# Optimization experiments

Measured on AMD Instinct MI355X. Metric: run time of the kernel, lower is better.

## Reference

```python
import jax, jax.numpy as jnp
import numpy as np

N_UE, N_AP, K = 8192, 2048, 3          # dst nodes, src nodes, neighbors per dst (graphlet_size-1)
E = N_UE * K
D_NODE, D_EDGE, H = 8, 4, 128          # raw feature dims, hidden_dim
PQC_DIM, PQC_OUT, NCLS = 2, 3, 2
NQ = 9                                  # 3 edge wires + 4 node wires (center=wire 3) + 2 ancilla (7,8)
CENTER = 3
C64 = jnp.complex64
X_GATE = jnp.array([[0.0, 1.0], [1.0, 0.0]], dtype=C64)


def RXm(t):
    c = jnp.cos(0.5 * t).astype(C64)
    s = (-1j * jnp.sin(0.5 * t)).astype(C64)
    return jnp.stack([jnp.stack([c, s]), jnp.stack([s, c])])


def RYm(t):
    c, s = jnp.cos(0.5 * t), jnp.sin(0.5 * t)
    return jnp.stack([jnp.stack([c, -s]), jnp.stack([s, c])]).astype(C64)


def RZm(t):
    e = jnp.exp(-0.5j * t.astype(C64))
    z = jnp.zeros_like(e)
    return jnp.stack([jnp.stack([e, z]), jnp.stack([z, jnp.conj(e)])])


def ROTm(phi, theta, omega):  # qml.Rot = RZ(omega) @ RY(theta) @ RZ(phi)
    return RZm(omega) @ RYm(theta) @ RZm(phi)


def ap1(psi, U, w):  # apply 1-qubit gate on wire w
    psi = jnp.tensordot(U, psi, axes=([1], [w]))
    return jnp.moveaxis(psi, 0, w)


def apc(psi, U, c, t):  # controlled-U, control c, target t
    G = jnp.zeros((4, 4), C64).at[:2, :2].set(jnp.eye(2, dtype=C64)).at[2:, 2:].set(U)
    psi = jnp.tensordot(G.reshape(2, 2, 2, 2), psi, axes=([2, 3], [c, t]))
    return jnp.moveaxis(psi, (0, 1), (c, t))


def sel(psi, w, wires):  # qml.StronglyEntanglingLayers, w: (L, M, 3)
    L, M = w.shape[0], len(wires)
    for l in range(L):
        for j, q in enumerate(wires):
            psi = ap1(psi, ROTm(w[l, j, 0], w[l, j, 1], w[l, j, 2]), q)
        r = l % (M - 1) + 1  # pennylane default ranges
        for j in range(M):
            psi = apc(psi, X_GATE, wires[j], wires[(j + r) % M])
    return psi


def expz(psi, w):  # <PauliZ(w)>
    p = psi.real ** 2 + psi.imag ** 2
    m = p.sum(axis=tuple(a for a in range(NQ) if a != w))
    return m[0] - m[1]


def circuit(flat, strong, inits, update):  # qgcn_enhance_layer, flat: (14,)
    inp = flat.reshape(7, 2)
    ef, nf = inp[:3], inp[3:]  # 3 edge rows, then center + 3 neighbor rows
    psi = jnp.zeros((2,) * NQ, C64).at[(0,) * NQ].set(1.0)
    for i in range(3):  # edge feature encoding
        psi = ap1(psi, RXm(ef[i, 0]), i)
        psi = ap1(psi, RZm(ef[i, 1]), i)
    for i in range(4):  # node feature encoding (center on wire 3)
        psi = ap1(psi, RXm(nf[i, 0]), CENTER + i)
        psi = ap1(psi, RZm(nf[i, 1]), CENTER + i)
    for i in range(3):  # message_passing_pqc per edge
        e, nb = i, CENTER + i + 1
        psi = apc(psi, RXm(inits[0, 0]), nb, e)
        psi = apc(psi, RYm(inits[0, 1]), e, nb)
        psi = sel(psi, strong[0], [e, nb])
    for i in range(3):  # update entanglers over center/neighbor/ancilla
        psi = sel(psi, update[i], [CENTER, CENTER + i + 1, 7, 8])
    return jnp.stack([expz(psi, CENTER), expz(psi, 7), expz(psi, 8)])


def mlp2(x, W1, b1, W2, b2):  # PyG MLP in eval mode; BatchNorm at default stats == identity
    return jax.nn.leaky_relu(x @ W1 + b1) @ W2 + b2


def _forward(x_ue, x_ap, edge_attr,
             Wn1u, bn1u, Wn2u, bn2u, Wn1a, bn1a, Wn2a, bn2a,
             We1, be1, We2, be2, strong, inits, update,
             Wu1, bu1, Wu2, bu2, ln_g, ln_b,
             Wf1, bf1, Wf2, bf2, Wf3, bf3, edge_src):
    ue = mlp2(x_ue, Wn1u, bn1u, Wn2u, bn2u)        # (N_UE, 2)  input_node['UE']
    ap = mlp2(x_ap, Wn1a, bn1a, Wn2a, bn2a)        # (N_AP, 2)  input_node['AP']
    ea = mlp2(edge_attr, We1, be1, We2, be2)       # (E, 2)     input_edge['UE']
    nbrs = ap[edge_src].reshape(N_UE, K, PQC_DIM)  # neighbor gather (K per dst)
    ef = ea.reshape(N_UE, K, PQC_DIM)              # edges grouped by dst: edge_dst = repeat(arange(N_UE), K)
    flat = jnp.concatenate([ef, ue[:, None, :], nbrs], axis=1).reshape(N_UE, 14)
    msg = jax.vmap(lambda f: circuit(f, strong, inits, update))(flat)  # (N_UE, 3)
    upd = mlp2(jnp.concatenate([ue, msg], axis=-1), Wu1, bu1, Wu2, bu2)  # (N_UE, 2)
    h = ue + upd  # index_add scatter: each dst updated exactly once
    mu = h.mean(-1, keepdims=True)
    var = h.var(-1, keepdims=True)
    h = (h - mu) / jnp.sqrt(var + 1e-5) * ln_g + ln_b  # LayerNorm(2)
    h = jax.nn.leaky_relu(h @ Wf1 + bf1)
    h = jax.nn.leaky_relu(h @ Wf2 + bf2)
    return jax.nn.sigmoid(h @ Wf3 + bf3)  # (N_UE, NCLS)


def setup_inputs() -> dict:
    ks = jax.random.split(jax.random.key(0), 20)

    def rn(i, shape, s=0.2):
        return jax.random.normal(ks[i], shape, jnp.float32) * s

    def qw(i, shape):  # uniform_pi_init
        return jax.random.uniform(ks[i], shape, jnp.float32, 0.0, np.pi)

    return dict(
        x_ue=jax.random.normal(ks[0], (N_UE, D_NODE), jnp.float32),
        x_ap=jax.random.normal(ks[1], (N_AP, D_NODE), jnp.float32),
        edge_attr=jax.random.normal(ks[2], (E, D_EDGE), jnp.float32),
        edge_src=jax.random.randint(ks[3], (E,), 0, N_AP),
        edge_dst=jnp.repeat(jnp.arange(N_UE), K),
        Wn1u=rn(4, (D_NODE, H)), bn1u=jnp.zeros((H,), jnp.float32),
        Wn2u=rn(5, (H, PQC_DIM)), bn2u=jnp.zeros((PQC_DIM,), jnp.float32),
        Wn1a=rn(6, (D_NODE, H)), bn1a=jnp.zeros((H,), jnp.float32),
        Wn2a=rn(7, (H, PQC_DIM)), bn2a=jnp.zeros((PQC_DIM,), jnp.float32),
        We1=rn(8, (D_EDGE, H)), be1=jnp.zeros((H,), jnp.float32),
        We2=rn(9, (H, PQC_DIM)), be2=jnp.zeros((PQC_DIM,), jnp.float32),
        strong=qw(10, (1, 2, 2, 3)), inits=qw(11, (1, 2)), update=qw(12, (3, 2, 4, 3)),
        Wu1=rn(13, (PQC_DIM + PQC_OUT, H)), bu1=jnp.zeros((H,), jnp.float32),
        Wu2=rn(14, (H, PQC_DIM)), bu2=jnp.zeros((PQC_DIM,), jnp.float32),
        ln_g=jnp.ones((PQC_DIM,), jnp.float32), ln_b=jnp.zeros((PQC_DIM,), jnp.float32),
        Wf1=rn(15, (PQC_DIM, H)), bf1=jnp.zeros((H,), jnp.float32),
        Wf2=rn(16, (H, H)), bf2=jnp.zeros((H,), jnp.float32),
        Wf3=rn(17, (H, NCLS)), bf3=jnp.zeros((NCLS,), jnp.float32),
    )


def reference(x_ue, x_ap, edge_attr, edge_src, edge_dst,
              Wn1u, bn1u, Wn2u, bn2u, Wn1a, bn1a, Wn2a, bn2a,
              We1, be1, We2, be2, strong, inits, update,
              Wu1, bu1, Wu2, bu2, ln_g, ln_b,
              Wf1, bf1, Wf2, bf2, Wf3, bf3):
    del edge_dst  # edges are constructed grouped per dst; grouping realized via reshape
    return _forward(x_ue, x_ap, edge_attr,
                    Wn1u, bn1u, Wn2u, bn2u, Wn1a, bn1a, Wn2a, bn2a,
                    We1, be1, We2, be2, strong, inits, update,
                    Wu1, bu1, Wu2, bu2, ln_g, ln_b,
                    Wf1, bf1, Wf2, bf2, Wf3, bf3, edge_src)
```

## Files before the change

kernel.cpp:

```cpp
#include <hip/hip_runtime.h>

#define LEAKY(x) ((x) > 0.0f ? (x) : 0.01f * (x))

#define GP_F    672
#define APE     2208
#define UEE     6304
#define EAE     22688
#define G_F     71840

__device__ __forceinline__ float2 cmul(float2 a, float2 b) {
  return make_float2(fmaf(a.x, b.x, -a.y * b.y), fmaf(a.x, b.y, a.y * b.x));
}
__device__ __forceinline__ float2 cmulc(float2 a, float2 b) {
  return make_float2(fmaf(a.x, b.x, a.y * b.y), fmaf(a.x, b.y, -a.y * b.x));
}
__device__ __forceinline__ float2 cadd(float2 a, float2 b) {
  return make_float2(a.x + b.x, a.y + b.y);
}
__device__ __forceinline__ float2 csub(float2 a, float2 b) {
  return make_float2(a.x - b.x, a.y - b.y);
}
__device__ __forceinline__ void swap2(float2& a, float2& b) {
  float2 t = a; a = b; b = t;
}

struct C2 { float2 e[4]; };

__device__ C2 cmm(const C2& A, const C2& B) {
  C2 R;
  #pragma unroll
  for (int r = 0; r < 2; ++r)
    #pragma unroll
    for (int c = 0; c < 2; ++c)
      R.e[r*2+c] = cadd(cmul(A.e[r*2+0], B.e[0*2+c]), cmul(A.e[r*2+1], B.e[1*2+c]));
  return R;
}
__device__ C2 gRX(float t) {
  float s = __sinf(0.5f*t), c = __cosf(0.5f*t);
  C2 M;
  M.e[0] = make_float2(c, 0.f);  M.e[1] = make_float2(0.f, -s);
  M.e[2] = make_float2(0.f, -s); M.e[3] = make_float2(c, 0.f);
  return M;
}
__device__ C2 gRY(float t) {
  float s = __sinf(0.5f*t), c = __cosf(0.5f*t);
  C2 M;
  M.e[0] = make_float2(c, 0.f);  M.e[1] = make_float2(-s, 0.f);
  M.e[2] = make_float2(s, 0.f);  M.e[3] = make_float2(c, 0.f);
  return M;
}
__device__ C2 gRZ(float t) {
  float s = __sinf(0.5f*t), c = __cosf(0.5f*t);
  C2 M;
  M.e[0] = make_float2(c, -s);    M.e[1] = make_float2(0.f, 0.f);
  M.e[2] = make_float2(0.f, 0.f); M.e[3] = make_float2(c, s);
  return M;
}
__device__ C2 gROT(float phi, float th, float om) {
  return cmm(cmm(gRZ(om), gRY(th)), gRZ(phi));
}

template<int D>
__device__ __forceinline__ void encode_block(
    const float* __restrict__ x, int r,
    const float* __restrict__ W1, const float* __restrict__ b1,
    const float* __restrict__ W2, const float* __restrict__ b2,
    float* w1t, float* b1s, float* w2s, float* __restrict__ outp, int tid) {
  #pragma unroll
  for (int i = 0; i < D/2; ++i) {
    const int idx = i*256 + tid;
    const float v = W1[idx];
    w1t[(idx & 127)*D + (idx >> 7)] = v;
  }
  if (tid < 128) b1s[tid] = b1[tid];
  w2s[tid] = W2[tid];
  __syncthreads();

  float xv[D];
  *(float4*)xv = *(const float4*)(x + r*D);
  if (D == 8) *(float4*)(xv + 4) = *(const float4*)(x + r*D + 4);

  float o0 = 0.f, o1 = 0.f;
  #pragma unroll 4
  for (int j = 0; j < 128; ++j) {
    float h = b1s[j];
    #pragma unroll
    for (int k = 0; k < D; k += 4) {
      const float4 w = *(const float4*)&w1t[j*D + k];
      h = fmaf(xv[k],   w.x, h);
      h = fmaf(xv[k+1], w.y, h);
      h = fmaf(xv[k+2], w.z, h);
      h = fmaf(xv[k+3], w.w, h);
    }
    h = LEAKY(h);
    const float2 w2 = *(const float2*)&w2s[j*2];
    o0 = fmaf(h, w2.x, o0);
    o1 = fmaf(h, w2.y, o1);
  }
  *(float2*)(outp + r*2) = make_float2(o0 + b2[0], o1 + b2[1]);
}

__global__ __launch_bounds__(256) void enc_kernel(
    const float* __restrict__ x_ue, const float* __restrict__ x_ap,
    const float* __restrict__ edge_attr,
    const float* __restrict__ Wn1u, const float* __restrict__ bn1u,
    const float* __restrict__ Wn2u, const float* __restrict__ bn2u,
    const float* __restrict__ Wn1a, const float* __restrict__ bn1a,
    const float* __restrict__ Wn2a, const float* __restrict__ bn2a,
    const float* __restrict__ We1,  const float* __restrict__ be1,
    const float* __restrict__ We2,  const float* __restrict__ be2,
    const float* __restrict__ strongp, const float* __restrict__ initsp,
    const float* __restrict__ updatep, float* __restrict__ ws) {
  __shared__ __align__(16) float w1t[1024];
  __shared__ float b1s[128];
  __shared__ __align__(8) float w2s[256];
  __shared__ float2 U2s[16][17];
  const int bi = blockIdx.x, tid = threadIdx.x;

  if (bi < 32) {
    encode_block<8>(x_ue, bi*256 + tid, Wn1u, bn1u, Wn2u, bn2u,
                    w1t, b1s, w2s, ws + UEE, tid);
    return;
  } else if (bi < 40) {
    encode_block<8>(x_ap, (bi-32)*256 + tid, Wn1a, bn1a, Wn2a, bn2a,
                    w1t, b1s, w2s, ws + APE, tid);
    return;
  } else if (bi < 136) {
    encode_block<4>(edge_attr, (bi-40)*256 + tid, We1, be1, We2, be2,
                    w1t, b1s, w2s, ws + EAE, tid);
    return;
  }

  if (tid < 48) {
    const int k = tid >> 4, col = tid & 15;
    float2 u[16];
    #pragma unroll
    for (int r = 0; r < 16; ++r) u[r] = make_float2(r == col ? 1.f : 0.f, 0.f);
    #pragma unroll
    for (int l = 0; l < 2; ++l) {
      #pragma unroll
      for (int j = 0; j < 4; ++j) {
        const float* p = updatep + k*24 + l*12 + j*3;
        C2 U = gROT(p[0], p[1], p[2]);
        const int m = 8 >> j;
        #pragma unroll
        for (int r = 0; r < 16; ++r)
          if (!(r & m)) {
            float2 a0 = u[r], a1 = u[r | m];
            u[r]     = cadd(cmul(U.e[0], a0), cmul(U.e[1], a1));
            u[r | m] = cadd(cmul(U.e[2], a0), cmul(U.e[3], a1));
          }
      }
      #pragma unroll
      for (int j = 0; j < 4; ++j) {
        const int mc = 8 >> j;
        const int mt0[4] = {4, 2, 1, 8};
        const int mt1[4] = {2, 1, 8, 4};
        const int mt = (l == 0) ? mt0[j] : mt1[j];
        #pragma unroll
        for (int r = 0; r < 16; ++r)
          if ((r & mc) && !(r & mt)) swap2(u[r], u[r | mt]);
      }
    }
    if (k == 0) {
      if (!(col & 3)) {
        const int jc = col >> 2;
        #pragma unroll
        for (int r = 0; r < 16; ++r) {
          ws[32 + (jc*16 + r)*2 + 0] = u[r].x;
          ws[32 + (jc*16 + r)*2 + 1] = u[r].y;
        }
      }
    } else if (k == 1) {
      #pragma unroll
      for (int r = 0; r < 16; ++r) {
        ws[160 + (col*16 + r)*2 + 0] = u[r].x;
        ws[160 + (col*16 + r)*2 + 1] = u[r].y;
      }
    } else {
      #pragma unroll
      for (int r = 0; r < 16; ++r) U2s[col][r] = u[r];
    }
  }
  if (tid == 48) {
    float2 M[4][4];
    #pragma unroll
    for (int r = 0; r < 4; ++r)
      #pragma unroll
      for (int c = 0; c < 4; ++c)
        M[r][c] = make_float2(r == c ? 1.f : 0.f, 0.f);
    auto rowpair = [&](int r0, int r1, C2 U) {
      #pragma unroll
      for (int c = 0; c < 4; ++c) {
        float2 a0 = M[r0][c], a1 = M[r1][c];
        M[r0][c] = cadd(cmul(U.e[0], a0), cmul(U.e[1], a1));
        M[r1][c] = cadd(cmul(U.e[2], a0), cmul(U.e[3], a1));
      }
    };
    auto rowswap = [&](int r0, int r1) {
      #pragma unroll
      for (int c = 0; c < 4; ++c) swap2(M[r0][c], M[r1][c]);
    };
    rowpair(1, 3, gRX(initsp[0]));
    rowpair(2, 3, gRY(initsp[1]));
    #pragma unroll
    for (int l = 0; l < 2; ++l) {
      C2 Re = gROT(strongp[l*6+0], strongp[l*6+1], strongp[l*6+2]);
      C2 Rn = gROT(strongp[l*6+3], strongp[l*6+4], strongp[l*6+5]);
      rowpair(0, 2, Re); rowpair(1, 3, Re);
      rowpair(0, 1, Rn); rowpair(2, 3, Rn);
      rowswap(2, 3);
      rowswap(1, 3);
    }
    #pragma unroll
    for (int r = 0; r < 4; ++r)
      #pragma unroll
      for (int c = 0; c < 4; ++c) {
        ws[(r*4 + c)*2 + 0] = M[r][c].x;
        ws[(r*4 + c)*2 + 1] = M[r][c].y;
      }
  }
  __syncthreads();
  {
    const int c = tid >> 5, cp = (tid >> 2) & 7, n = (tid >> 1) & 1, np = tid & 1;
    const int q  = ((c  & 4) << 1) | (n  << 2) | (c  & 3);
    const int qp = ((cp & 4) << 1) | (np << 2) | (cp & 3);
    float2 g3 = make_float2(0,0), g7 = g3, g8 = g3;
    #pragma unroll
    for (int t = 0; t < 16; ++t) {
      float2 pr = cmulc(U2s[q][t], U2s[qp][t]);
      g3 = (t & 8) ? csub(g3, pr) : cadd(g3, pr);
      g7 = (t & 2) ? csub(g7, pr) : cadd(g7, pr);
      g8 = (t & 1) ? csub(g8, pr) : cadd(g8, pr);
    }
    const int idx = (c*2 + n)*16 + (cp*2 + np);
    ws[GP_F + (0*256 + idx)*2 + 0] = g3.x;
    ws[GP_F + (0*256 + idx)*2 + 1] = g3.y;
    ws[GP_F + (1*256 + idx)*2 + 0] = g7.x;
    ws[GP_F + (1*256 + idx)*2 + 1] = g7.y;
    ws[GP_F + (2*256 + idx)*2 + 0] = g8.x;
    ws[GP_F + (2*256 + idx)*2 + 1] = g8.y;
  }
}

__global__ __launch_bounds__(256) void circuit_kernel(
    float* __restrict__ ws, const int* __restrict__ esrc,
    const float* __restrict__ Wu1, const float* __restrict__ bu1,
    const float* __restrict__ Wu2, const float* __restrict__ bu2,
    const float* __restrict__ lng, const float* __restrict__ lnb) {
  __shared__ __align__(16) float2 cst[1104];
  __shared__ __align__(16) float2 pr_s[4][3][4];
  __shared__ __align__(16) float2 psi0[4][2][16];
  __shared__ __align__(16) float2 psi2[4][8][16];
  const int tid = threadIdx.x, wv = tid >> 6, lane = tid & 63;
  const int u = blockIdx.x*4 + wv;

  {
    const float4* s4 = (const float4*)ws;
    float4* d4 = (float4*)cst;
    #pragma unroll
    for (int i = tid; i < 552; i += 256) d4[i] = s4[i];
  }
  __syncthreads();

  const float2* MEl  = cst;
  const float2* U0cl = cst + 16;
  const float2* U1tl = cst + 80;
  const float2* GPl  = cst + 336;

  auto mkv = [](float aa, float bb, float2& v0, float2& v1) {
    const float sa = __sinf(0.5f*aa), ca = __cosf(0.5f*aa);
    const float sb = __sinf(0.5f*bb), cb = __cosf(0.5f*bb);
    v0 = make_float2(cb*ca, -sb*ca);
    v1 = make_float2(sa*sb, -sa*cb);
  };
  const float2 ue_ab = *(const float2*)(ws + UEE + u*2);
  float2 t0, t1;
  mkv(ue_ab.x, ue_ab.y, t0, t1);

  if (lane < 12) {
    const int i = lane >> 2, r = lane & 3;
    const float2 eab = *(const float2*)(ws + EAE + (u*3 + i)*2);
    const int s = esrc[u*3 + i];
    const float2 nab = *(const float2*)(ws + APE + s*2);
    float2 e0, e1, n0, n1;
    mkv(eab.x, eab.y, e0, e1);
    mkv(nab.x, nab.y, n0, n1);
    float2 in4[4] = {cmul(e0,n0), cmul(e0,n1), cmul(e1,n0), cmul(e1,n1)};
    float2 acc = make_float2(0.f, 0.f);
    #pragma unroll
    for (int cc = 0; cc < 4; ++cc) acc = cadd(acc, cmul(MEl[r*4 + cc], in4[cc]));
    pr_s[wv][i][r] = acc;
  }

  if (lane < 32) {
    const int b = lane >> 4, row = lane & 15;
    float2 acc = make_float2(0.f, 0.f);
    #pragma unroll
    for (int j = 0; j < 4; ++j) {
      const float2 phi = pr_s[wv][0][(b << 1) | (j & 1)];
      const float2 coef = cmul((j >> 1) ? t1 : t0, phi);
      acc = cadd(acc, cmul(U0cl[j*16 + row], coef));
    }
    psi0[wv][b][row] = acc;
  }

  {
    const int ibr = lane >> 3, rp = lane & 7;
    const int db = ibr >> 2, da = (ibr >> 1) & 1, dbp = ibr & 1;
    const float2 f10 = pr_s[wv][1][(dbp << 1) | 0];
    const float2 f11 = pr_s[wv][1][(dbp << 1) | 1];
    float2 chi[8];
    {
      const float4 a0 = *(const float4*)&psi0[wv][db][da*4 + 0];
      const float4 a1 = *(const float4*)&psi0[wv][db][da*4 + 2];
      const float4 a2 = *(const float4*)&psi0[wv][db][8 + da*4 + 0];
      const float4 a3 = *(const float4*)&psi0[wv][db][8 + da*4 + 2];
      chi[0] = make_float2(a0.x, a0.y); chi[1] = make_float2(a0.z, a0.w);
      chi[2] = make_float2(a1.x, a1.y); chi[3] = make_float2(a1.z, a1.w);
      chi[4] = make_float2(a2.x, a2.y); chi[5] = make_float2(a2.z, a2.w);
      chi[6] = make_float2(a3.x, a3.y); chi[7] = make_float2(a3.z, a3.w);
    }
    float2 q0 = make_float2(0.f, 0.f), q1 = q0;
    #pragma unroll
    for (int q = 0; q < 16; ++q) {
      const int cc = ((q >> 3) << 2) | (q & 3);
      const float2 xq = cmul(chi[cc], (q & 4) ? f11 : f10);
      q0 = cadd(q0, cmul(U1tl[q*16 + rp],     xq));
      q1 = cadd(q1, cmul(U1tl[q*16 + rp + 8], xq));
    }
    psi2[wv][ibr][rp]     = q0;
    psi2[wv][ibr][rp + 8] = q1;
  }

  const int c = lane >> 3, cp = lane & 7;
  const int mc0 = ((c  & 4) << 1) | (c  & 3);
  const int mp0 = ((cp & 4) << 1) | (cp & 3);
  float2 R = make_float2(0.f, 0.f);
  #pragma unroll
  for (int br = 0; br < 8; ++br) {
    const float2 z10 = psi2[wv][br][mc0], z11 = psi2[wv][br][mc0 + 4];
    const float2 z20 = psi2[wv][br][mp0], z21 = psi2[wv][br][mp0 + 4];
    R.x += z10.x*z20.x + z10.y*z20.y + z11.x*z21.x + z11.y*z21.y;
    R.y += z10.y*z20.x - z10.x*z20.y + z11.y*z21.x - z11.x*z21.y;
  }

  const float4 f2a = *(const float4*)&pr_s[wv][2][0];
  const float4 f2b = *(const float4*)&pr_s[wv][2][2];
  const float2 f20 = make_float2(f2a.x, f2a.y), f21 = make_float2(f2a.z, f2a.w);
  const float2 f22 = make_float2(f2b.x, f2b.y), f23 = make_float2(f2b.z, f2b.w);
  const float2 rho00 = make_float2(f20.x*f20.x + f20.y*f20.y + f22.x*f22.x + f22.y*f22.y, 0.f);
  const float2 rho11 = make_float2(f21.x*f21.x + f21.y*f21.y + f23.x*f23.x + f23.y*f23.y, 0.f);
  const float2 rho01 = make_float2(fmaf(f20.x,f21.x,f20.y*f21.y) + fmaf(f22.x,f23.x,f22.y*f23.y),
                                   (f20.y*f21.x - f20.x*f21.y) + (f22.y*f23.x - f22.x*f23.y));
  const float2 rho10 = make_float2(rho01.x, -rho01.y);

  float ev0, ev1, ev2;
  {
    const int base = (c*2)*16 + (cp*2);
    #pragma unroll
    for (int w = 0; w < 3; ++w) {
      const float2 g00 = GPl[w*256 + base];
      const float2 g01 = GPl[w*256 + base + 1];
      const float2 g10 = GPl[w*256 + base + 16];
      const float2 g11 = GPl[w*256 + base + 17];
      float2 K = cmul(g00, rho00);
      K = cadd(K, cmul(g01, rho10));
      K = cadd(K, cmul(g10, rho01));
      K = cadd(K, cmul(g11, rho11));
      const float e = K.x*R.x + K.y*R.y;
      if (w == 0) ev0 = e; else if (w == 1) ev1 = e; else ev2 = e;
    }
  }
  #pragma unroll
  for (int o = 32; o; o >>= 1) {
    ev0 += __shfl_xor(ev0, o);
    ev1 += __shfl_xor(ev1, o);
    ev2 += __shfl_xor(ev2, o);
  }

  const int j1 = lane, j2 = lane + 64;
  const float in5[5] = {ue_ab.x, ue_ab.y, ev0, ev1, ev2};
  float h1 = bu1[j1], h2 = bu1[j2];
  #pragma unroll
  for (int k = 0; k < 5; ++k) {
    h1 = fmaf(in5[k], Wu1[k*128 + j1], h1);
    h2 = fmaf(in5[k], Wu1[k*128 + j2], h2);
  }
  h1 = LEAKY(h1); h2 = LEAKY(h2);
  const float2 wu2a = *(const float2*)(Wu2 + j1*2);
  const float2 wu2b = *(const float2*)(Wu2 + j2*2);
  float p0 = fmaf(h1, wu2a.x, h2*wu2b.x);
  float p1 = fmaf(h1, wu2a.y, h2*wu2b.y);
  #pragma unroll
  for (int o = 32; o; o >>= 1) { p0 += __shfl_xor(p0, o); p1 += __shfl_xor(p1, o); }
  if (lane == 0) {
    const float hh0 = ue_ab.x + p0 + bu2[0];
    const float hh1 = ue_ab.y + p1 + bu2[1];
    const float mu = 0.5f*(hh0 + hh1);
    const float dd = hh0 - mu;
    const float inv = rsqrtf(dd*dd + 1e-5f);
    const float g0 =  dd*inv*lng[0] + lnb[0];
    const float g1 = -dd*inv*lng[1] + lnb[1];
    *(float2*)(ws + G_F + u*2) = make_float2(g0, g1);
  }
}

__global__ __launch_bounds__(256) void head_kernel(
    const float* __restrict__ g,
    const float* __restrict__ Wf1, const float* __restrict__ bf1,
    const float* __restrict__ Wf2, const float* __restrict__ bf2,
    const float* __restrict__ Wf3, const float* __restrict__ bf3,
    float* __restrict__ out) {
  __shared__ float act[16][128];
  const int tid = threadIdx.x;
  const int rl = tid >> 4, sub = tid & 15;
  const int r = blockIdx.x*16 + rl;
  const float2 gv = *(const float2*)(g + r*2);
  {
    const float4 wa0 = ((const float4*)Wf1)[sub*2],       wa1 = ((const float4*)Wf1)[sub*2 + 1];
    const float4 wb0 = ((const float4*)(Wf1+128))[sub*2], wb1 = ((const float4*)(Wf1+128))[sub*2 + 1];
    const float4 bb0 = ((const float4*)bf1)[sub*2],       bb1 = ((const float4*)bf1)[sub*2 + 1];
    float4 a0, a1;
    a0.x = LEAKY(fmaf(gv.x, wa0.x, fmaf(gv.y, wb0.x, bb0.x)));
    a0.y = LEAKY(fmaf(gv.x, wa0.y, fmaf(gv.y, wb0.y, bb0.y)));
    a0.z = LEAKY(fmaf(gv.x, wa0.z, fmaf(gv.y, wb0.z, bb0.z)));
    a0.w = LEAKY(fmaf(gv.x, wa0.w, fmaf(gv.y, wb0.w, bb0.w)));
    a1.x = LEAKY(fmaf(gv.x, wa1.x, fmaf(gv.y, wb1.x, bb1.x)));
    a1.y = LEAKY(fmaf(gv.x, wa1.y, fmaf(gv.y, wb1.y, bb1.y)));
    a1.z = LEAKY(fmaf(gv.x, wa1.z, fmaf(gv.y, wb1.z, bb1.z)));
    a1.w = LEAKY(fmaf(gv.x, wa1.w, fmaf(gv.y, wb1.w, bb1.w)));
    *(float4*)&act[rl][sub*8]     = a0;
    *(float4*)&act[rl][sub*8 + 4] = a1;
  }
  __syncthreads();
  float h2[8];
  {
    const float4 c0 = ((const float4*)bf2)[sub*2], c1 = ((const float4*)bf2)[sub*2 + 1];
    h2[0]=c0.x; h2[1]=c0.y; h2[2]=c0.z; h2[3]=c0.w;
    h2[4]=c1.x; h2[5]=c1.y; h2[6]=c1.z; h2[7]=c1.w;
  }
  #pragma unroll 4
  for (int k = 0; k < 128; ++k) {
    const float a = act[rl][k];
    const float4 w0 = ((const float4*)(Wf2 + k*128))[sub*2];
    const float4 w1 = ((const float4*)(Wf2 + k*128))[sub*2 + 1];
    h2[0] = fmaf(a, w0.x, h2[0]); h2[1] = fmaf(a, w0.y, h2[1]);
    h2[2] = fmaf(a, w0.z, h2[2]); h2[3] = fmaf(a, w0.w, h2[3]);
    h2[4] = fmaf(a, w1.x, h2[4]); h2[5] = fmaf(a, w1.y, h2[5]);
    h2[6] = fmaf(a, w1.z, h2[6]); h2[7] = fmaf(a, w1.w, h2[7]);
  }
  float p0 = 0.f, p1 = 0.f;
  {
    const float4 w3a = ((const float4*)Wf3)[sub*4 + 0];
    const float4 w3b = ((const float4*)Wf3)[sub*4 + 1];
    const float4 w3c = ((const float4*)Wf3)[sub*4 + 2];
    const float4 w3d = ((const float4*)Wf3)[sub*4 + 3];
    const float v0 = LEAKY(h2[0]), v1 = LEAKY(h2[1]), v2 = LEAKY(h2[2]), v3 = LEAKY(h2[3]);
    const float v4 = LEAKY(h2[4]), v5 = LEAKY(h2[5]), v6 = LEAKY(h2[6]), v7 = LEAKY(h2[7]);
    p0 = v0*w3a.x + v1*w3a.z + v2*w3b.x + v3*w3b.z + v4*w3c.x + v5*w3c.z + v6*w3d.x + v7*w3d.z;
    p1 = v0*w3a.y + v1*w3a.w + v2*w3b.y + v3*w3b.w + v4*w3c.y + v5*w3c.w + v6*w3d.y + v7*w3d.w;
  }
  #pragma unroll
  for (int o = 8; o; o >>= 1) { p0 += __shfl_xor(p0, o); p1 += __shfl_xor(p1, o); }
  if (sub == 0) {
    const float s0 = 1.f/(1.f + __expf(-(p0 + bf3[0])));
    const float s1 = 1.f/(1.f + __expf(-(p1 + bf3[1])));
    *(float2*)(out + r*2) = make_float2(s0, s1);
  }
}

extern "C" void kernel_launch(void* const* d_in, const int* in_sizes, int n_in,
                              void* d_out, int out_size, void* d_ws, size_t ws_size,
                              hipStream_t stream) {
  (void)in_sizes; (void)n_in; (void)out_size; (void)ws_size;
  const float* x_ue      = (const float*)d_in[0];
  const float* x_ap      = (const float*)d_in[1];
  const float* edge_attr = (const float*)d_in[2];
  const int*   edge_src  = (const int*)d_in[3];
  const float* Wn1u = (const float*)d_in[5];
  const float* bn1u = (const float*)d_in[6];
  const float* Wn2u = (const float*)d_in[7];
  const float* bn2u = (const float*)d_in[8];
  const float* Wn1a = (const float*)d_in[9];
  const float* bn1a = (const float*)d_in[10];
  const float* Wn2a = (const float*)d_in[11];
  const float* bn2a = (const float*)d_in[12];
  const float* We1  = (const float*)d_in[13];
  const float* be1  = (const float*)d_in[14];
  const float* We2  = (const float*)d_in[15];
  const float* be2  = (const float*)d_in[16];
  const float* strong = (const float*)d_in[17];
  const float* inits  = (const float*)d_in[18];
  const float* update = (const float*)d_in[19];
  const float* Wu1  = (const float*)d_in[20];
  const float* bu1  = (const float*)d_in[21];
  const float* Wu2  = (const float*)d_in[22];
  const float* bu2  = (const float*)d_in[23];
  const float* ln_g = (const float*)d_in[24];
  const float* ln_b = (const float*)d_in[25];
  const float* Wf1  = (const float*)d_in[26];
  const float* bf1  = (const float*)d_in[27];
  const float* Wf2  = (const float*)d_in[28];
  const float* bf2  = (const float*)d_in[29];
  const float* Wf3  = (const float*)d_in[30];
  const float* bf3  = (const float*)d_in[31];

  float* ws = (float*)d_ws;

  enc_kernel<<<137, 256, 0, stream>>>(x_ue, x_ap, edge_attr,
                                      Wn1u, bn1u, Wn2u, bn2u,
                                      Wn1a, bn1a, Wn2a, bn2a,
                                      We1, be1, We2, be2,
                                      strong, inits, update, ws);
  circuit_kernel<<<2048, 256, 0, stream>>>(ws, edge_src,
                                           Wu1, bu1, Wu2, bu2, ln_g, ln_b);
  head_kernel<<<512, 256, 0, stream>>>(ws + G_F, Wf1, bf1, Wf2, bf2, Wf3, bf3,
                                       (float*)d_out);
}
```

Measured before the change: 41.61 us.

## Register-tile head MLP over 64 rows per block to reuse Wf2 loads

The head kernel now processes 64 rows per block instead of 16. Each thread computes a 4-row by 8-column register tile, reading the first-layer activations from a transposed shared-memory buffer. Each Wf2 load is therefore reused across four rows, cutting global/L2 weight traffic by about 4x. In exchange the grid drops to 128 blocks, which lowers parallelism on a GPU with many CUs, and per-thread register use goes up.

```diff
diff --git a/kernel.cpp b/kernel.cpp
--- a/kernel.cpp
+++ b/kernel.cpp
@@ -412,61 +412,86 @@
     const float* __restrict__ Wf2, const float* __restrict__ bf2,
     const float* __restrict__ Wf3, const float* __restrict__ bf3,
     float* __restrict__ out) {
-  __shared__ float act[16][128];
+  __shared__ __align__(16) float act_t[128][64];
   const int tid = threadIdx.x;
-  const int rl = tid >> 4, sub = tid & 15;
-  const int r = blockIdx.x*16 + rl;
-  const float2 gv = *(const float2*)(g + r*2);
+  const int r0 = blockIdx.x * 64;
+  const int wv = tid >> 6;
+
   {
-    const float4 wa0 = ((const float4*)Wf1)[sub*2],       wa1 = ((const float4*)Wf1)[sub*2 + 1];
-    const float4 wb0 = ((const float4*)(Wf1+128))[sub*2], wb1 = ((const float4*)(Wf1+128))[sub*2 + 1];
-    const float4 bb0 = ((const float4*)bf1)[sub*2],       bb1 = ((const float4*)bf1)[sub*2 + 1];
-    float4 a0, a1;
-    a0.x = LEAKY(fmaf(gv.x, wa0.x, fmaf(gv.y, wb0.x, bb0.x)));
-    a0.y = LEAKY(fmaf(gv.x, wa0.y, fmaf(gv.y, wb0.y, bb0.y)));
-    a0.z = LEAKY(fmaf(gv.x, wa0.z, fmaf(gv.y, wb0.z, bb0.z)));
-    a0.w = LEAKY(fmaf(gv.x, wa0.w, fmaf(gv.y, wb0.w, bb0.w)));
-    a1.x = LEAKY(fmaf(gv.x, wa1.x, fmaf(gv.y, wb1.x, bb1.x)));
-    a1.y = LEAKY(fmaf(gv.x, wa1.y, fmaf(gv.y, wb1.y, bb1.y)));
-    a1.z = LEAKY(fmaf(gv.x, wa1.z, fmaf(gv.y, wb1.z, bb1.z)));
-    a1.w = LEAKY(fmaf(gv.x, wa1.w, fmaf(gv.y, wb1.w, bb1.w)));
-    *(float4*)&act[rl][sub*8]     = a0;
-    *(float4*)&act[rl][sub*8 + 4] = a1;
+    const int row = tid & 63;
+    const float2 gv = *(const float2*)(g + (r0 + row)*2);
+    #pragma unroll
+    for (int p = 0; p < 32; ++p) {
+      const int j = p*4 + wv;
+      act_t[j][row] = LEAKY(fmaf(gv.x, Wf1[j], fmaf(gv.y, Wf1[128 + j], bf1[j])));
+    }
   }
   __syncthreads();
-  float h2[8];
+
+  const int cg = tid & 15, rg = tid >> 4;
+  float acc[4][8];
   {
-    const float4 c0 = ((const float4*)bf2)[sub*2], c1 = ((const float4*)bf2)[sub*2 + 1];
-    h2[0]=c0.x; h2[1]=c0.y; h2[2]=c0.z; h2[3]=c0.w;
-    h2[4]=c1.x; h2[5]=c1.y; h2[6]=c1.z; h2[7]=c1.w;
+    const float4 b0 = *(const float4*)(bf2 + cg*8);
+    const float4 b1 = *(const float4*)(bf2 + cg*8 + 4);
+    #pragma unroll
+    for (int r = 0; r < 4; ++r) {
+      acc[r][0]=b0.x; acc[r][1]=b0.y; acc[r][2]=b0.z; acc[r][3]=b0.w;
+      acc[r][4]=b1.x; acc[r][5]=b1.y; acc[r][6]=b1.z; acc[r][7]=b1.w;
+    }
   }
   #pragma unroll 4
   for (int k = 0; k < 128; ++k) {
-    const float a = act[rl][k];
-    const float4 w0 = ((const float4*)(Wf2 + k*128))[sub*2];
-    const float4 w1 = ((const float4*)(Wf2 + k*128))[sub*2 + 1];
-    h2[0] = fmaf(a, w0.x, h2[0]); h2[1] = fmaf(a, w0.y, h2[1]);
-    h2[2] = fmaf(a, w0.z, h2[2]); h2[3] = fmaf(a, w0.w, h2[3]);
-    h2[4] = fmaf(a, w1.x, h2[4]); h2[5] = fmaf(a, w1.y, h2[5]);
-    h2[6] = fmaf(a, w1.z, h2[6]); h2[7] = fmaf(a, w1.w, h2[7]);
-  }
-  float p0 = 0.f, p1 = 0.f;
-  {
-    const float4 w3a = ((const float4*)Wf3)[sub*4 + 0];
-    const float4 w3b = ((const float4*)Wf3)[sub*4 + 1];
-    const float4 w3c = ((const float4*)Wf3)[sub*4 + 2];
-    const float4 w3d = ((const float4*)Wf3)[sub*4 + 3];
-    const float v0 = LEAKY(h2[0]), v1 = LEAKY(h2[1]), v2 = LEAKY(h2[2]), v3 = LEAKY(h2[3]);
-    const float v4 = LEAKY(h2[4]), v5 = LEAKY(h2[5]), v6 = LEAKY(h2[6]), v7 = LEAKY(h2[7]);
-    p0 = v0*w3a.x + v1*w3a.z + v2*w3b.x + v3*w3b.z + v4*w3c.x + v5*w3c.z + v6*w3d.x + v7*w3d.z;
-    p1 = v0*w3a.y + v1*w3a.w + v2*w3b.y + v3*w3b.w + v4*w3c.y + v5*w3c.w + v6*w3d.y + v7*w3d.w;
-  }
-  #pragma unroll
-  for (int o = 8; o; o >>= 1) { p0 += __shfl_xor(p0, o); p1 += __shfl_xor(p1, o); }
-  if (sub == 0) {
-    const float s0 = 1.f/(1.f + __expf(-(p0 + bf3[0])));
-    const float s1 = 1.f/(1.f + __expf(-(p1 + bf3[1])));
-    *(float2*)(out + r*2) = make_float2(s0, s1);
+    const float4 a4 = *(const float4*)&act_t[k][rg*4];
+    const float4 w0 = *(const float4*)(Wf2 + k*128 + cg*8);
+    const float4 w1 = *(const float4*)(Wf2 + k*128 + cg*8 + 4);
+    const float av[4] = {a4.x, a4.y, a4.z, a4.w};
+    #pragma unroll
+    for (int r = 0; r < 4; ++r) {
+      acc[r][0] = fmaf(av[r], w0.x, acc[r][0]);
+      acc[r][1] = fmaf(av[r], w0.y, acc[r][1]);
+      acc[r][2] = fmaf(av[r], w0.z, acc[r][2]);
+      acc[r][3] = fmaf(av[r], w0.w, acc[r][3]);
+      acc[r][4] = fmaf(av[r], w1.x, acc[r][4]);
+      acc[r][5] = fmaf(av[r], w1.y, acc[r][5]);
+      acc[r][6] = fmaf(av[r], w1.z, acc[r][6]);
+      acc[r][7] = fmaf(av[r], w1.w, acc[r][7]);
+    }
+  }
+
+  float w3x[8], w3y[8];
+  #pragma unroll
+  for (int c = 0; c < 8; ++c) {
+    const float2 w3 = *(const float2*)(Wf3 + (cg*8 + c)*2);
+    w3x[c] = w3.x; w3y[c] = w3.y;
+  }
+  float p0[4], p1[4];
+  #pragma unroll
+  for (int r = 0; r < 4; ++r) {
+    float s0 = 0.f, s1 = 0.f;
+    #pragma unroll
+    for (int c = 0; c < 8; ++c) {
+      const float v = LEAKY(acc[r][c]);
+      s0 = fmaf(v, w3x[c], s0);
+      s1 = fmaf(v, w3y[c], s1);
+    }
+    p0[r] = s0; p1[r] = s1;
+  }
+  #pragma unroll
+  for (int o = 8; o; o >>= 1) {
+    #pragma unroll
+    for (int r = 0; r < 4; ++r) {
+      p0[r] += __shfl_xor(p0[r], o);
+      p1[r] += __shfl_xor(p1[r], o);
+    }
+  }
+  if (cg == 0) {
+    #pragma unroll
+    for (int r = 0; r < 4; ++r) {
+      const int row = r0 + rg*4 + r;
+      const float s0 = 1.f/(1.f + __expf(-(p0[r] + bf3[0])));
+      const float s1 = 1.f/(1.f + __expf(-(p1[r] + bf3[1])));
+      *(float2*)(out + row*2) = make_float2(s0, s1);
+    }
   }
 }
 
@@ -515,6 +540,6 @@
                                       strong, inits, update, ws);
   circuit_kernel<<<2048, 256, 0, stream>>>(ws, edge_src,
                                            Wu1, bu1, Wu2, bu2, ln_g, ln_b);
-  head_kernel<<<512, 256, 0, stream>>>(ws + G_F, Wf1, bf1, Wf2, bf2, Wf3, bf3,
+  head_kernel<<<128, 256, 0, stream>>>(ws + G_F, Wf1, bf1, Wf2, bf2, Wf3, bf3,
                                        (float*)d_out);
 }
```

After: 37.99 us. 1.1x faster.
